# Kernel optimization log

Hardware: AMD Instinct MI355X
Metric: run time of the kernel (lower is better)

Reference implementation:

```python
import jax, jax.numpy as jnp
import numpy as np
from math import sqrt

W_SIZE = jnp.array([32, 64, 128, 256, 32, 64, 128, 256], dtype=jnp.int32)  # per-head window

def setup_inputs() -> dict:
    key = jax.random.key(0)
    kq, kk, kv = jax.random.split(key, 3)
    B, L, H, E = 4, 2048, 8, 64
    D = 64
    return {
        "queries": jax.random.normal(kq, (B, L, H, E), dtype=jnp.float32),
        "keys": jax.random.normal(kk, (B, L, H, E), dtype=jnp.float32),
        "values": jax.random.normal(kv, (B, L, H, D), dtype=jnp.float32),
    }

def reference(queries, keys, values):
    B, L, H, E = queries.shape
    scale = 1.0 / sqrt(E)
    # dense scores: [B, H, L, L]
    scores = jnp.einsum('blhe,bshe->bhls', queries, keys)
    # per-head band mask: |i - j| <= w[h]  -> [H, L, L]
    i = jnp.arange(L)
    diff = jnp.abs(i[:, None] - i[None, :])            # [L, L]
    band = diff[None, :, :] <= W_SIZE[:, None, None]   # [H, L, L]
    scores = jnp.where(band[None], scores, -jnp.inf)
    A = jax.nn.softmax(scale * scores, axis=-1)        # dropout p=0 (eval)
    V = jnp.einsum('bhls,bshd->blhd', A, values)
    return V
```

## Files before the change

kernel.cpp:

```cpp
#include <hip/hip_runtime.h>
#include <math.h>


#define LL 2048
#define HH 8
#define EE 64
#define DD 64
#define RS (HH * EE)

typedef __attribute__((ext_vector_type(8))) short short8;
typedef __attribute__((ext_vector_type(4))) float floatx4;
typedef __attribute__((ext_vector_type(4))) _Float16 half4;
typedef __attribute__((ext_vector_type(2))) __fp16 fp16x2;

static __device__ __forceinline__ unsigned f2bf(float f) {
    union { float f; unsigned u; } v; v.f = f;
    return (v.u + 0x7fff + ((v.u >> 16) & 1)) >> 16;
}
static __device__ __forceinline__ unsigned pack2(float a, float b) {
    return f2bf(a) | (f2bf(b) << 16);
}
static __device__ __forceinline__ unsigned packh2(float a, float b) {
    union { fp16x2 h; unsigned u; } v;
    v.h = __builtin_amdgcn_cvt_pkrtz(a, b);
    return v.u;
}

#define K_BUF(cu)  (sAll + (cu) * 4096)
#define V_BUF(cu)  (sAll + 8192 + (cu) * 4608)

__global__ __launch_bounds__(512, 4) void mwa_r9(
    const float* __restrict__ Q,
    const float* __restrict__ K,
    const float* __restrict__ V,
    float* __restrict__ O)
{
    const int tid  = threadIdx.x;
    const int lane = tid & 63;
    const int wv   = tid >> 6;
    const int quad = lane >> 4;
    const int l15  = lane & 15;

    const int gid   = blockIdx.x;
    const int heavy = (gid >> 8) == 0;
    const int c     = gid & 255;
    const int it    = c >> 4;
    const int rem   = c & 15;
    const int b     = rem >> 2;
    const int z     = rem & 3;
    const int hb    = z >> 1;
    const int p     = z & 1;
    const int h     = hb * 4 + (heavy ? (3 - p) : p);
    const int i0    = it << 7;
    const int w     = 32 << (h & 3);

    alignas(16) __shared__ short sAll[17408];

    const float* Qb = Q + ((size_t)b * LL * HH + h) * EE;
    const float* Kb = K + ((size_t)b * LL * HH + h) * EE;
    const float* Vb = V + ((size_t)b * LL * HH + h) * DD;
    float*       Ob = O + ((size_t)b * LL * HH + h) * DD;

    {
        const float sc = 0.125f;
        const int row = tid >> 2, cc = (tid & 3) << 4;
        const float4* src = (const float4*)(Qb + (size_t)(i0 + row) * RS + cc);
        float4 f0 = src[0], f1 = src[1], f2 = src[2], f3 = src[3];
        uint4 u0 = { pack2(sc*f0.x,sc*f0.y), pack2(sc*f0.z,sc*f0.w),
                     pack2(sc*f1.x,sc*f1.y), pack2(sc*f1.z,sc*f1.w) };
        uint4 u1 = { pack2(sc*f2.x,sc*f2.y), pack2(sc*f2.z,sc*f2.w),
                     pack2(sc*f3.x,sc*f3.y), pack2(sc*f3.z,sc*f3.w) };
        uint4* dst = (uint4*)&sAll[row * 72 + cc];
        dst[0] = u0; dst[1] = u1;
    }
    __syncthreads();
    short8 qf0, qf1;
    {
        const short* qp = &sAll[(wv * 16 + l15) * 72 + quad * 8];
        qf0 = *(const short8*)qp;
        qf1 = *(const short8*)(qp + 32);
    }
    __syncthreads();

    const int jt_lo = max(0, i0 - w) >> 6;
    const int jt_hi = min(LL - 1, i0 + 127 + w) >> 6;

    {
        const int j0 = jt_lo << 6;
        const int row = tid >> 3, cc = (tid & 7) << 3;
        const float4* src = (const float4*)(Kb + (size_t)(j0 + row) * RS + cc);
        float4 f0 = src[0], f1 = src[1];
        float vv[8];
#pragma unroll
        for (int rr = 0; rr < 8; ++rr)
            vv[rr] = Vb[(size_t)(j0 + wv * 8 + rr) * RS + lane];

        uint4 u0 = { pack2(f0.x,f0.y), pack2(f0.z,f0.w), pack2(f1.x,f1.y), pack2(f1.z,f1.w) };
        const int jtw = row >> 4, l15w = row & 15, ks = cc >> 5, q0 = (cc >> 3) & 3;
        *(uint4*)&K_BUF(0)[(((jtw * 2 + ks) * 4 + q0) * 16 + l15w) * 8] = u0;

        uint4 w0 = { packh2(vv[0],vv[1]), packh2(vv[2],vv[3]),
                     packh2(vv[4],vv[5]), packh2(vv[6],vv[7]) };
        *(uint4*)&V_BUF(0)[lane * 72 + wv * 8] = w0;
    }
    __syncthreads();

    floatx4 acc[4] = {};
    float lsum = 0.f;
    const int iq = i0 + wv * 16 + l15;

    for (int jt = jt_lo; jt <= jt_hi; ++jt) {
        const int cur = (jt - jt_lo) & 1;
        const int nxt = cur ^ 1;
        const bool more = jt < jt_hi;
        const int j0 = jt << 6;

        float4 kf0, kf1;
        float vv[8];
        const int rowp = tid >> 3, cp = (tid & 7) << 3;
        if (more) {
            const int jn = (jt + 1) << 6;
            const float4* src = (const float4*)(Kb + (size_t)(jn + rowp) * RS + cp);
            kf0 = src[0]; kf1 = src[1];
#pragma unroll
            for (int rr = 0; rr < 8; ++rr)
                vv[rr] = Vb[(size_t)(jn + wv * 8 + rr) * RS + lane];
        }

        const bool full = ((i0 + 127 - j0) <= w) && ((j0 + 63 - i0) <= w);
        half4 pf[4];
#pragma unroll
        for (int t4 = 0; t4 < 4; ++t4) {
            const short* kp = &K_BUF(cur)[1024 * t4 + 128 * quad + 8 * l15];
            short8 k0 = *(const short8*)kp;
            short8 k1 = *(const short8*)(kp + 512);
            floatx4 st = {};
            st = __builtin_amdgcn_mfma_f32_16x16x32_bf16(k0, qf0, st, 0, 0, 0);
            st = __builtin_amdgcn_mfma_f32_16x16x32_bf16(k1, qf1, st, 0, 0, 0);

            float pr[4];
            const int jb = j0 + t4 * 16 + quad * 4;
#pragma unroll
            for (int r = 0; r < 4; ++r) {
                float x = st[r];
                if (!full) {
                    const int di = iq - (jb + r);
                    x = (di <= w && di >= -w) ? x : -INFINITY;
                }
                pr[r] = __expf(x);
                lsum += pr[r];
            }
            union { half4 v; unsigned u[2]; } pu;
            pu.u[0] = packh2(pr[0], pr[1]);
            pu.u[1] = packh2(pr[2], pr[3]);
            pf[t4] = pu.v;
        }

#pragma unroll
        for (int nt = 0; nt < 4; ++nt) {
            const short* vbase = &V_BUF(cur)[(nt * 16 + l15) * 72];
#pragma unroll
            for (int t4 = 0; t4 < 4; ++t4) {
                half4 vf = *(const half4*)(vbase + t4 * 16 + quad * 4);
                acc[nt] = __builtin_amdgcn_mfma_f32_16x16x16f16(pf[t4], vf, acc[nt], 0, 0, 0);
            }
        }

        if (more) {
            uint4 u0 = { pack2(kf0.x,kf0.y), pack2(kf0.z,kf0.w),
                         pack2(kf1.x,kf1.y), pack2(kf1.z,kf1.w) };
            const int jtw = rowp >> 4, l15w = rowp & 15, ks = cp >> 5, q0 = (cp >> 3) & 3;
            *(uint4*)&K_BUF(nxt)[(((jtw * 2 + ks) * 4 + q0) * 16 + l15w) * 8] = u0;

            uint4 w0 = { packh2(vv[0],vv[1]), packh2(vv[2],vv[3]),
                         packh2(vv[4],vv[5]), packh2(vv[6],vv[7]) };
            *(uint4*)&V_BUF(nxt)[lane * 72 + wv * 8] = w0;
        }
        __syncthreads();
    }

    lsum += __shfl_xor(lsum, 16, 64);
    lsum += __shfl_xor(lsum, 32, 64);
    float rinv[4];
#pragma unroll
    for (int r = 0; r < 4; ++r) {
        const float lr = __shfl(lsum, quad * 4 + r, 64);
        rinv[r] = 1.0f / lr;
    }
#pragma unroll
    for (int nt = 0; nt < 4; ++nt) {
#pragma unroll
        for (int r = 0; r < 4; ++r) {
            Ob[(size_t)(i0 + wv * 16 + quad * 4 + r) * RS + nt * 16 + l15]
                = acc[nt][r] * rinv[r];
        }
    }
}

extern "C" void kernel_launch(void* const* d_in, const int* in_sizes, int n_in,
                              void* d_out, int out_size, void* d_ws, size_t ws_size,
                              hipStream_t stream)
{
    const float* Q = (const float*)d_in[0];
    const float* K = (const float*)d_in[1];
    const float* V = (const float*)d_in[2];
    float* O = (float*)d_out;

    dim3 grid(512), block(512);
    hipLaunchKernelGGL(mwa_r9, grid, block, 0, stream, Q, K, V, O);
}
```

Measured before the change: 101.6 us.

## Deepen global prefetch to two tiles and skip out-of-band 16-key subtiles per wave

The key loop is unrolled by two with two register sets, so global loads for K/V run two tiles ahead of compute instead of one, which should hide more memory latency. Each wave now checks every 16-key subtile against its own 16-query band and skips the QK MFMAs, exp and PV MFMAs for subtiles that lie entirely outside the window. Masking is applied per subtile rather than per whole tile. The extra prefetch register set raises register pressure under the 512-thread, 4-block launch bound and may cause spills.

```diff
diff --git a/kernel.cpp b/kernel.cpp
--- a/kernel.cpp
+++ b/kernel.cpp
@@ -29,7 +29,71 @@
 #define K_BUF(cu)  (sAll + (cu) * 4096)
 #define V_BUF(cu)  (sAll + 8192 + (cu) * 4608)
 
-__global__ __launch_bounds__(512, 4) void mwa_r9(
+static __device__ __forceinline__ void compute_tile(
+    int j0, const short* __restrict__ kbase, const short* __restrict__ vbase,
+    int w, int qb, int iq, int quad, int l15,
+    short8 qf0, short8 qf1, floatx4* __restrict__ acc, float& lsum)
+{
+#pragma unroll
+    for (int t4 = 0; t4 < 4; ++t4) {
+        const int jb = j0 + t4 * 16;
+        if (jb > qb + 15 + w || jb + 15 < qb - w) continue;
+        const bool needMask = ((jb + 15 - qb) > w) || ((qb + 15 - jb) > w);
+
+        const short* kp = kbase + 1024 * t4 + 128 * quad + 8 * l15;
+        short8 k0 = *(const short8*)kp;
+        short8 k1 = *(const short8*)(kp + 512);
+        floatx4 st = {};
+        st = __builtin_amdgcn_mfma_f32_16x16x32_bf16(k0, qf0, st, 0, 0, 0);
+        st = __builtin_amdgcn_mfma_f32_16x16x32_bf16(k1, qf1, st, 0, 0, 0);
+
+        float pr[4];
+        const int jq = jb + quad * 4;
+#pragma unroll
+        for (int r = 0; r < 4; ++r) {
+            float x = st[r];
+            if (needMask) {
+                const int di = iq - (jq + r);
+                x = (di <= w && di >= -w) ? x : -INFINITY;
+            }
+            pr[r] = __expf(x);
+            lsum += pr[r];
+        }
+        half4 pf;
+        {
+            union { half4 v; unsigned u[2]; } pu;
+            pu.u[0] = packh2(pr[0], pr[1]);
+            pu.u[1] = packh2(pr[2], pr[3]);
+            pf = pu.v;
+        }
+#pragma unroll
+        for (int nt = 0; nt < 4; ++nt) {
+            half4 vf = *(const half4*)(vbase + (nt * 16 + l15) * 72 + t4 * 16 + quad * 4);
+            acc[nt] = __builtin_amdgcn_mfma_f32_16x16x16f16(pf, vf, acc[nt], 0, 0, 0);
+        }
+    }
+}
+
+#define ISSUE(jn, kf0_, kf1_, vv_)                                              \
+    {                                                                           \
+        const float4* src_ = (const float4*)(Kb + (size_t)((jn) + rowp) * RS + cp); \
+        kf0_ = src_[0]; kf1_ = src_[1];                                         \
+        _Pragma("unroll")                                                       \
+        for (int rr_ = 0; rr_ < 8; ++rr_)                                       \
+            vv_[rr_] = Vb[(size_t)((jn) + wv * 8 + rr_) * RS + lane];           \
+    }
+
+#define STAGE(bufIdx, kf0_, kf1_, vv_)                                          \
+    {                                                                           \
+        uint4 u0_ = { pack2(kf0_.x,kf0_.y), pack2(kf0_.z,kf0_.w),               \
+                      pack2(kf1_.x,kf1_.y), pack2(kf1_.z,kf1_.w) };             \
+        *(uint4*)&K_BUF(bufIdx)[kWoff] = u0_;                                   \
+        uint4 w0_ = { packh2(vv_[0],vv_[1]), packh2(vv_[2],vv_[3]),             \
+                      packh2(vv_[4],vv_[5]), packh2(vv_[6],vv_[7]) };           \
+        *(uint4*)&V_BUF(bufIdx)[vWoff] = w0_;                                   \
+    }
+
+__global__ __launch_bounds__(512, 4) void mwa_r10(
     const float* __restrict__ Q,
     const float* __restrict__ K,
     const float* __restrict__ V,
@@ -84,99 +148,38 @@
 
     const int jt_lo = max(0, i0 - w) >> 6;
     const int jt_hi = min(LL - 1, i0 + 127 + w) >> 6;
-
-    {
-        const int j0 = jt_lo << 6;
-        const int row = tid >> 3, cc = (tid & 7) << 3;
-        const float4* src = (const float4*)(Kb + (size_t)(j0 + row) * RS + cc);
-        float4 f0 = src[0], f1 = src[1];
-        float vv[8];
-#pragma unroll
-        for (int rr = 0; rr < 8; ++rr)
-            vv[rr] = Vb[(size_t)(j0 + wv * 8 + rr) * RS + lane];
-
-        uint4 u0 = { pack2(f0.x,f0.y), pack2(f0.z,f0.w), pack2(f1.x,f1.y), pack2(f1.z,f1.w) };
-        const int jtw = row >> 4, l15w = row & 15, ks = cc >> 5, q0 = (cc >> 3) & 3;
-        *(uint4*)&K_BUF(0)[(((jtw * 2 + ks) * 4 + q0) * 16 + l15w) * 8] = u0;
-
-        uint4 w0 = { packh2(vv[0],vv[1]), packh2(vv[2],vv[3]),
-                     packh2(vv[4],vv[5]), packh2(vv[6],vv[7]) };
-        *(uint4*)&V_BUF(0)[lane * 72 + wv * 8] = w0;
-    }
+    const int n     = jt_hi - jt_lo + 1;
+
+    const int rowp  = tid >> 3, cp = (tid & 7) << 3;
+    const int jtw   = rowp >> 4, l15w = rowp & 15, ks = cp >> 5, q0w = (cp >> 3) & 3;
+    const int kWoff = (((jtw * 2 + ks) * 4 + q0w) * 16 + l15w) * 8;
+    const int vWoff = lane * 72 + wv * 8;
+
+    float4 kA0, kA1; float vA[8];
+    float4 kB0, kB1; float vB[8];
+    ISSUE(jt_lo << 6, kA0, kA1, vA);
+    STAGE(0, kA0, kA1, vA);
     __syncthreads();
+    if (n > 1) ISSUE((jt_lo + 1) << 6, kA0, kA1, vA);
 
     floatx4 acc[4] = {};
     float lsum = 0.f;
     const int iq = i0 + wv * 16 + l15;
-
-    for (int jt = jt_lo; jt <= jt_hi; ++jt) {
-        const int cur = (jt - jt_lo) & 1;
-        const int nxt = cur ^ 1;
-        const bool more = jt < jt_hi;
-        const int j0 = jt << 6;
-
-        float4 kf0, kf1;
-        float vv[8];
-        const int rowp = tid >> 3, cp = (tid & 7) << 3;
-        if (more) {
-            const int jn = (jt + 1) << 6;
-            const float4* src = (const float4*)(Kb + (size_t)(jn + rowp) * RS + cp);
-            kf0 = src[0]; kf1 = src[1];
-#pragma unroll
-            for (int rr = 0; rr < 8; ++rr)
-                vv[rr] = Vb[(size_t)(jn + wv * 8 + rr) * RS + lane];
-        }
-
-        const bool full = ((i0 + 127 - j0) <= w) && ((j0 + 63 - i0) <= w);
-        half4 pf[4];
-#pragma unroll
-        for (int t4 = 0; t4 < 4; ++t4) {
-            const short* kp = &K_BUF(cur)[1024 * t4 + 128 * quad + 8 * l15];
-            short8 k0 = *(const short8*)kp;
-            short8 k1 = *(const short8*)(kp + 512);
-            floatx4 st = {};
-            st = __builtin_amdgcn_mfma_f32_16x16x32_bf16(k0, qf0, st, 0, 0, 0);
-            st = __builtin_amdgcn_mfma_f32_16x16x32_bf16(k1, qf1, st, 0, 0, 0);
-
-            float pr[4];
-            const int jb = j0 + t4 * 16 + quad * 4;
-#pragma unroll
-            for (int r = 0; r < 4; ++r) {
-                float x = st[r];
-                if (!full) {
-                    const int di = iq - (jb + r);
-                    x = (di <= w && di >= -w) ? x : -INFINITY;
-                }
-                pr[r] = __expf(x);
-                lsum += pr[r];
-            }
-            union { half4 v; unsigned u[2]; } pu;
-            pu.u[0] = packh2(pr[0], pr[1]);
-            pu.u[1] = packh2(pr[2], pr[3]);
-            pf[t4] = pu.v;
-        }
-
-#pragma unroll
-        for (int nt = 0; nt < 4; ++nt) {
-            const short* vbase = &V_BUF(cur)[(nt * 16 + l15) * 72];
-#pragma unroll
-            for (int t4 = 0; t4 < 4; ++t4) {
-                half4 vf = *(const half4*)(vbase + t4 * 16 + quad * 4);
-                acc[nt] = __builtin_amdgcn_mfma_f32_16x16x16f16(pf[t4], vf, acc[nt], 0, 0, 0);
-            }
-        }
-
-        if (more) {
-            uint4 u0 = { pack2(kf0.x,kf0.y), pack2(kf0.z,kf0.w),
-                         pack2(kf1.x,kf1.y), pack2(kf1.z,kf1.w) };
-            const int jtw = rowp >> 4, l15w = rowp & 15, ks = cp >> 5, q0 = (cp >> 3) & 3;
-            *(uint4*)&K_BUF(nxt)[(((jtw * 2 + ks) * 4 + q0) * 16 + l15w) * 8] = u0;
-
-            uint4 w0 = { packh2(vv[0],vv[1]), packh2(vv[2],vv[3]),
-                         packh2(vv[4],vv[5]), packh2(vv[6],vv[7]) };
-            *(uint4*)&V_BUF(nxt)[lane * 72 + wv * 8] = w0;
-        }
+    const int qb = i0 + wv * 16;
+
+    for (int s = 0; s < n; s += 2) {
+        const int jt = jt_lo + s;
+        if (s + 2 < n) ISSUE((jt + 2) << 6, kB0, kB1, vB);
+        compute_tile(jt << 6, K_BUF(0), V_BUF(0), w, qb, iq, quad, l15, qf0, qf1, acc, lsum);
+        if (s + 1 < n) STAGE(1, kA0, kA1, vA);
         __syncthreads();
+
+        if (s + 1 < n) {
+            if (s + 3 < n) ISSUE((jt + 3) << 6, kA0, kA1, vA);
+            compute_tile((jt + 1) << 6, K_BUF(1), V_BUF(1), w, qb, iq, quad, l15, qf0, qf1, acc, lsum);
+            if (s + 2 < n) STAGE(0, kB0, kB1, vB);
+            __syncthreads();
+        }
     }
 
     lsum += __shfl_xor(lsum, 16, 64);
@@ -207,5 +210,5 @@
     float* O = (float*)d_out;
 
     dim3 grid(512), block(512);
-    hipLaunchKernelGGL(mwa_r9, grid, block, 0, stream, Q, K, V, O);
-}
+    hipLaunchKernelGGL(mwa_r10, grid, block, 0, stream, Q, K, V, O);
+}
```

New measurement: 100.9 us. No clear change (-0.7%).
